# Performance work log

Measured on AMD Instinct MI355X. Metric: run time of the kernel, lower is better.

Reference implementation:

```python
import jax, jax.numpy as jnp
import numpy as np

NUM_EXPERTS = 8
HIDDEN = 1024
FFN = 2048
TOKENS = 2048


def setup_inputs() -> dict:
    key = jax.random.key(0)
    k_x, k_idx, k_w1, k_w2 = jax.random.split(key, 4)
    scale = 0.02
    x = jax.random.normal(k_x, (TOKENS, HIDDEN), dtype=jnp.float32)
    expert_indices = jax.random.randint(k_idx, (TOKENS,), 0, NUM_EXPERTS, dtype=jnp.int64)
    W1 = jax.random.normal(k_w1, (NUM_EXPERTS, HIDDEN, FFN), dtype=jnp.float32) * scale
    b1 = jnp.zeros((NUM_EXPERTS, FFN), dtype=jnp.float32)
    W2 = jax.random.normal(k_w2, (NUM_EXPERTS, FFN, HIDDEN), dtype=jnp.float32) * scale
    b2 = jnp.zeros((NUM_EXPERTS, HIDDEN), dtype=jnp.float32)
    return {"x": x, "expert_indices": expert_indices, "W1": W1, "b1": b1, "W2": W2, "b2": b2}


def reference(x, expert_indices, W1, b1, W2, b2):
    # Each token routed to one expert's MLP: Linear -> GELU(exact) -> Linear.
    # Dropout is identity in eval mode. Loop is over the small fixed expert set.
    out = jnp.zeros_like(x)
    for e in range(NUM_EXPERTS):
        h = jax.nn.gelu(x @ W1[e] + b1[e], approximate=False)  # [T, FFN]
        y = h @ W2[e] + b2[e]                                   # [T, H]
        mask = (expert_indices == e)[:, None]
        out = out + jnp.where(mask, y, 0.0)
    return out
```

## Files before the change

kernel.cpp:

```cpp
#include <hip/hip_runtime.h>

#define T_TOK 2048
#define HID   1024
#define FFN   2048
#define NEXP  8
#define MAX_SLOTS 40

typedef __attribute__((ext_vector_type(8))) short bf16x8;
typedef __attribute__((ext_vector_type(4))) float f32x4;

__device__ __forceinline__ short f2bf(float f) {
    unsigned u = __builtin_bit_cast(unsigned, f);
    u = (u + 0x7fffu + ((u >> 16) & 1u)) >> 16;
    return (short)u;
}

__device__ __forceinline__ float gelu_exact(float x) {
    return 0.5f * x * (1.0f + erff(x * 0.70710678118654752f));
}

__device__ __forceinline__ void async_cp16(const short* g, short* l) {
    __builtin_amdgcn_global_load_lds(
        (const __attribute__((address_space(1))) unsigned int*)g,
        (__attribute__((address_space(3))) unsigned int*)l, 16, 0, 0);
}

__device__ __forceinline__ void wtrans_body(
        const float* __restrict__ W, short* __restrict__ WT,
        int K, int N, int e, int kblk, int nblk) {
    int tid = threadIdx.x;
    int w = tid >> 6, l = tid & 63;
    int kb = kblk * 32 + w * 8;
    int n4 = nblk * 256 + l * 4;
    const float* src = W + (size_t)e * K * N + (size_t)kb * N + n4;
    float4 v[8];
#pragma unroll
    for (int r = 0; r < 8; r++)
        v[r] = *(const float4*)(src + (size_t)r * N);
    int kpanel = kb >> 6;
    int kc = (kb >> 3) & 7;
    int npanel = n4 >> 7;
    int n_in = n4 & 127;
    int kpanels = K >> 6;
    short* dst = WT + (size_t)e * K * N
               + ((size_t)npanel * kpanels + kpanel) * 8192
               + kc * 1024 + n_in * 8;
#pragma unroll
    for (int j = 0; j < 4; j++) {
        bf16x8 o = {f2bf(((const float*)&v[0])[j]), f2bf(((const float*)&v[1])[j]),
                    f2bf(((const float*)&v[2])[j]), f2bf(((const float*)&v[3])[j]),
                    f2bf(((const float*)&v[4])[j]), f2bf(((const float*)&v[5])[j]),
                    f2bf(((const float*)&v[6])[j]), f2bf(((const float*)&v[7])[j])};
        *(bf16x8*)(dst + j * 8) = o;
    }
}

__global__ __launch_bounds__(256) void prep_kernel(
        const float* __restrict__ x, const int* __restrict__ idx,
        const float* __restrict__ b2,
        const float* __restrict__ W1, const float* __restrict__ W2,
        short* __restrict__ xb, float* __restrict__ out,
        short* __restrict__ W1T, short* __restrict__ W2T,
        int* __restrict__ offs, int* __restrict__ cnts,
        int* __restrict__ tokl,
        int* __restrict__ slot_e, int* __restrict__ slot_t0) {
    int bx = blockIdx.x;
    int tid = threadIdx.x;
    if (bx < 2048) {
        int e = bx >> 8, rem = bx & 255;
        wtrans_body(W1, W1T, HID, FFN, e, rem & 31, rem >> 5);
    } else if (bx < 4096) {
        int b = bx - 2048;
        int e = b >> 8, rem = b & 255;
        wtrans_body(W2, W2T, FFN, HID, e, rem & 63, rem >> 6);
    } else if (bx < 5120) {
        int i = ((bx - 4096) * 256 + tid) * 8;
        float4 v0 = *(const float4*)(x + i);
        float4 v1 = *(const float4*)(x + i + 4);
        bf16x8 r = {f2bf(v0.x), f2bf(v0.y), f2bf(v0.z), f2bf(v0.w),
                    f2bf(v1.x), f2bf(v1.y), f2bf(v1.z), f2bf(v1.w)};
        *(bf16x8*)(xb + i) = r;
    } else if (bx < 7168) {
        int t = bx - 5120;
        int e = idx[t];
        ((float4*)(out + (size_t)t * HID))[tid] =
            ((const float4*)(b2 + (size_t)e * HID))[tid];
    } else {
        __shared__ int c[NEXP], cur[NEXP], o[NEXP];
        if (tid < NEXP) { c[tid] = 0; cur[tid] = 0; }
        __syncthreads();
        for (int t = tid; t < T_TOK; t += 256) atomicAdd(&c[idx[t]], 1);
        __syncthreads();
        if (tid == 0) {
            int s = 0;
            for (int e = 0; e < NEXP; e++) { o[e] = s; s += c[e]; }
            int ns = 0;
            for (int e = 0; e < NEXP; e++)
                for (int t0 = 0; t0 < c[e]; t0 += 64) {
                    slot_e[ns] = e; slot_t0[ns] = t0; ns++;
                }
            for (; ns < MAX_SLOTS; ns++) slot_e[ns] = -1;
        }
        __syncthreads();
        if (tid < NEXP) { offs[tid] = o[tid]; cnts[tid] = c[tid]; }
        for (int t = tid; t < T_TOK; t += 256) {
            int e = idx[t];
            int p = o[e] + atomicAdd(&cur[e], 1);
            tokl[p] = t;
        }
    }
}

__global__ __launch_bounds__(256) void gemm1_kernel(
        const short* __restrict__ xb, const short* __restrict__ W1T,
        const float* __restrict__ b1,
        const int* __restrict__ offs, const int* __restrict__ cnts,
        const int* __restrict__ tokl,
        const int* __restrict__ slot_e, const int* __restrict__ slot_t0,
        short* __restrict__ hg) {
    int s = blockIdx.y;
    int e = slot_e[s];
    if (e < 0) return;
    int t0 = slot_t0[s], count = cnts[e], off = offs[e];
    int n0 = blockIdx.x * 128;

    __shared__ short As[2 * 64 * 64];
    __shared__ short Bs[2 * 8 * 128 * 8];
    __shared__ int stok[64];

    int tid = threadIdx.x;
    if (tid < 64) {
        int p = t0 + tid;
        stok[tid] = tokl[off + (p < count ? p : count - 1)];
    }
    __syncthreads();

    int w = tid >> 6, l = tid & 63, l15 = l & 15, quad = l >> 4;
    int wm = (w >> 1) * 32, wn = (w & 1) * 64;

    int m0 = w * 16 + (l >> 3), m1 = m0 + 8;
    int cs = l & 7;
    int c0 = (cs - m0) & 7, c1 = (cs - m1) & 7;
    const short* gA0 = xb + (size_t)stok[m0] * HID + c0 * 8;
    const short* gA1 = xb + (size_t)stok[m1] * HID + c1 * 8;
    int aoff = w * 1024 + l * 8;

    const short* Bpan = W1T + (size_t)e * (HID * FFN)
                      + (size_t)(n0 >> 7) * ((HID >> 6) * 8192);
    int bo0 = (2 * w) * 1024 + l * 8;
    int bo1 = bo0 + 1024;
    int bo2 = bo0 + 512;
    int bo3 = bo1 + 512;

    auto stage = [&](int buf, int kt) {
        const short* bp = Bpan + (size_t)kt * 8192;
        short* As_b = As + buf * 4096;
        short* Bs_b = Bs + buf * 8192;
        async_cp16(gA0, As_b + aoff);
        async_cp16(gA1, As_b + aoff + 512);
        async_cp16(bp + bo0, Bs_b + bo0);
        async_cp16(bp + bo1, Bs_b + bo1);
        async_cp16(bp + bo2, Bs_b + bo2);
        async_cp16(bp + bo3, Bs_b + bo3);
        gA0 += 64; gA1 += 64;
    };

    f32x4 acc[2][4];
#pragma unroll
    for (int i = 0; i < 2; i++)
#pragma unroll
        for (int j = 0; j < 4; j++) acc[i][j] = (f32x4){0.f, 0.f, 0.f, 0.f};

    stage(0, 0);
    __syncthreads();

    const int KT = HID / 64;
    for (int kt = 0; kt < KT; kt++) {
        if (kt + 1 < KT) stage((kt + 1) & 1, kt + 1);
        const short* As_b = As + (kt & 1) * 4096;
        const short* Bs_b = Bs + (kt & 1) * 8192;
        bf16x8 a[2][2], b[2][4];
#pragma unroll
        for (int kk = 0; kk < 2; kk++) {
#pragma unroll
            for (int mt = 0; mt < 2; mt++) {
                int m = wm + mt * 16 + l15;
                a[kk][mt] = *(const bf16x8*)&As_b[m * 64 + (((kk * 4 + quad) + m) & 7) * 8];
            }
#pragma unroll
            for (int nt = 0; nt < 4; nt++) {
                int n = wn + nt * 16 + l15;
                b[kk][nt] = *(const bf16x8*)&Bs_b[(kk * 4 + quad) * 1024 + n * 8];
            }
        }
#pragma unroll
        for (int kk = 0; kk < 2; kk++)
#pragma unroll
            for (int mt = 0; mt < 2; mt++)
#pragma unroll
                for (int nt = 0; nt < 4; nt++)
                    acc[mt][nt] = __builtin_amdgcn_mfma_f32_16x16x32_bf16(
                        a[kk][mt], b[kk][nt], acc[mt][nt], 0, 0, 0);
        __syncthreads();
    }

    const float* b1e = b1 + e * FFN + n0;
#pragma unroll
    for (int mt = 0; mt < 2; mt++) {
        int rbase = wm + mt * 16 + quad * 4;
#pragma unroll
        for (int nt = 0; nt < 4; nt++) {
            int coln = wn + nt * 16 + l15;
            float bb = b1e[coln];
#pragma unroll
            for (int r = 0; r < 4; r++) {
                int p = t0 + rbase + r;
                if (p < count)
                    hg[(size_t)(off + p) * FFN + n0 + coln] =
                        f2bf(gelu_exact(acc[mt][nt][r] + bb));
            }
        }
    }
}

__global__ __launch_bounds__(256) void gemm2_kernel(
        const short* __restrict__ hg, const short* __restrict__ W2T,
        const int* __restrict__ offs, const int* __restrict__ cnts,
        const int* __restrict__ tokl,
        const int* __restrict__ slot_e, const int* __restrict__ slot_t0,
        float* __restrict__ out) {
    int s = blockIdx.y;
    int e = slot_e[s];
    if (e < 0) return;
    int t0 = slot_t0[s], count = cnts[e], off = offs[e];
    int ks = blockIdx.z;
    int n0 = blockIdx.x * 128;

    __shared__ short As[2 * 64 * 64];
    __shared__ short Bs[2 * 8 * 128 * 8];
    __shared__ int stok[64];

    int tid = threadIdx.x;
    if (tid < 64) {
        int p = t0 + tid;
        stok[tid] = tokl[off + (p < count ? p : count - 1)];
    }
    __syncthreads();

    int w = tid >> 6, l = tid & 63, l15 = l & 15, quad = l >> 4;
    int wm = (w >> 1) * 32, wn = (w & 1) * 64;

    int m0 = w * 16 + (l >> 3), m1 = m0 + 8;
    int cs = l & 7;
    int c0 = (cs - m0) & 7, c1 = (cs - m1) & 7;
    int g0 = off + (t0 + m0 < count ? t0 + m0 : count - 1);
    int g1 = off + (t0 + m1 < count ? t0 + m1 : count - 1);
    const short* gA0 = hg + (size_t)g0 * FFN + ks * 1024 + c0 * 8;
    const short* gA1 = hg + (size_t)g1 * FFN + ks * 1024 + c1 * 8;
    int aoff = w * 1024 + l * 8;

    const short* Bpan = W2T + (size_t)e * (FFN * HID)
                      + (size_t)(n0 >> 7) * ((FFN >> 6) * 8192)
                      + (size_t)ks * 16 * 8192;
    int bo0 = (2 * w) * 1024 + l * 8;
    int bo1 = bo0 + 1024;
    int bo2 = bo0 + 512;
    int bo3 = bo1 + 512;

    auto stage = [&](int buf, int kt) {
        const short* bp = Bpan + (size_t)kt * 8192;
        short* As_b = As + buf * 4096;
        short* Bs_b = Bs + buf * 8192;
        async_cp16(gA0, As_b + aoff);
        async_cp16(gA1, As_b + aoff + 512);
        async_cp16(bp + bo0, Bs_b + bo0);
        async_cp16(bp + bo1, Bs_b + bo1);
        async_cp16(bp + bo2, Bs_b + bo2);
        async_cp16(bp + bo3, Bs_b + bo3);
        gA0 += 64; gA1 += 64;
    };

    f32x4 acc[2][4];
#pragma unroll
    for (int i = 0; i < 2; i++)
#pragma unroll
        for (int j = 0; j < 4; j++) acc[i][j] = (f32x4){0.f, 0.f, 0.f, 0.f};

    stage(0, 0);
    __syncthreads();

    const int KT = 16;
    for (int kt = 0; kt < KT; kt++) {
        if (kt + 1 < KT) stage((kt + 1) & 1, kt + 1);
        const short* As_b = As + (kt & 1) * 4096;
        const short* Bs_b = Bs + (kt & 1) * 8192;
        bf16x8 a[2][2], b[2][4];
#pragma unroll
        for (int kk = 0; kk < 2; kk++) {
#pragma unroll
            for (int mt = 0; mt < 2; mt++) {
                int m = wm + mt * 16 + l15;
                a[kk][mt] = *(const bf16x8*)&As_b[m * 64 + (((kk * 4 + quad) + m) & 7) * 8];
            }
#pragma unroll
            for (int nt = 0; nt < 4; nt++) {
                int n = wn + nt * 16 + l15;
                b[kk][nt] = *(const bf16x8*)&Bs_b[(kk * 4 + quad) * 1024 + n * 8];
            }
        }
#pragma unroll
        for (int kk = 0; kk < 2; kk++)
#pragma unroll
            for (int mt = 0; mt < 2; mt++)
#pragma unroll
                for (int nt = 0; nt < 4; nt++)
                    acc[mt][nt] = __builtin_amdgcn_mfma_f32_16x16x32_bf16(
                        a[kk][mt], b[kk][nt], acc[mt][nt], 0, 0, 0);
        __syncthreads();
    }

#pragma unroll
    for (int mt = 0; mt < 2; mt++) {
        int rbase = wm + mt * 16 + quad * 4;
#pragma unroll
        for (int nt = 0; nt < 4; nt++) {
            int coln = n0 + wn + nt * 16 + l15;
#pragma unroll
            for (int r = 0; r < 4; r++) {
                int p = t0 + rbase + r;
                if (p < count) {
                    int tok = stok[rbase + r];
                    atomicAdd(out + (size_t)tok * HID + coln, acc[mt][nt][r]);
                }
            }
        }
    }
}

extern "C" void kernel_launch(void* const* d_in, const int* in_sizes, int n_in,
                              void* d_out, int out_size, void* d_ws, size_t ws_size,
                              hipStream_t stream) {
    const float* x   = (const float*)d_in[0];
    const int*   idx = (const int*)d_in[1];
    const float* W1  = (const float*)d_in[2];
    const float* b1  = (const float*)d_in[3];
    const float* W2  = (const float*)d_in[4];
    const float* b2  = (const float*)d_in[5];
    float* out = (float*)d_out;

    const size_t META = 32768;
    int*   offs    = (int*)d_ws;
    int*   cnts    = offs + 8;
    int*   tokl    = offs + 16;
    int*   slot_e  = offs + 16 + T_TOK;
    int*   slot_t0 = slot_e + MAX_SLOTS;
    char*  base    = (char*)d_ws + META;
    short* xb  = (short*)base;
    short* hg  = (short*)(base + (size_t)T_TOK * HID * 2);
    short* W1T = (short*)(base + (size_t)T_TOK * HID * 2 + (size_t)T_TOK * FFN * 2);
    short* W2T = W1T + (size_t)NEXP * FFN * HID;

    prep_kernel<<<7169, 256, 0, stream>>>(
        x, idx, b2, W1, W2, xb, out, W1T, W2T,
        offs, cnts, tokl, slot_e, slot_t0);

    gemm1_kernel<<<dim3(FFN / 128, MAX_SLOTS), 256, 0, stream>>>(
        xb, W1T, b1, offs, cnts, tokl, slot_e, slot_t0, hg);
    gemm2_kernel<<<dim3(HID / 128, MAX_SLOTS, 2), 256, 0, stream>>>(
        hg, W2T, offs, cnts, tokl, slot_e, slot_t0, out);
}
```

Baseline: 230.1 us.

## Pre-gather sorted tokens, overlap W2 conversion with GEMM1, relax pipeline waits

```diff
diff --git a/kernel.cpp b/kernel.cpp
--- a/kernel.cpp
+++ b/kernel.cpp
@@ -55,97 +55,103 @@
     }
 }
 
-__global__ __launch_bounds__(256) void prep_kernel(
-        const float* __restrict__ x, const int* __restrict__ idx,
-        const float* __restrict__ b2,
-        const float* __restrict__ W1, const float* __restrict__ W2,
-        short* __restrict__ xb, float* __restrict__ out,
-        short* __restrict__ W1T, short* __restrict__ W2T,
+__global__ __launch_bounds__(256) void bucket_kernel(
+        const int* __restrict__ idx,
         int* __restrict__ offs, int* __restrict__ cnts,
         int* __restrict__ tokl,
         int* __restrict__ slot_e, int* __restrict__ slot_t0) {
+    int tid = threadIdx.x;
+    __shared__ int c[NEXP], cur[NEXP], o[NEXP];
+    if (tid < NEXP) { c[tid] = 0; cur[tid] = 0; }
+    __syncthreads();
+    for (int t = tid; t < T_TOK; t += 256) atomicAdd(&c[idx[t]], 1);
+    __syncthreads();
+    if (tid == 0) {
+        int s = 0;
+        for (int e = 0; e < NEXP; e++) { o[e] = s; s += c[e]; }
+        int ns = 0;
+        for (int e = 0; e < NEXP; e++)
+            for (int t0 = 0; t0 < c[e]; t0 += 64) {
+                slot_e[ns] = e; slot_t0[ns] = t0; ns++;
+            }
+        for (; ns < MAX_SLOTS; ns++) slot_e[ns] = -1;
+    }
+    __syncthreads();
+    if (tid < NEXP) { offs[tid] = o[tid]; cnts[tid] = c[tid]; }
+    for (int t = tid; t < T_TOK; t += 256) {
+        int e = idx[t];
+        int p = o[e] + atomicAdd(&cur[e], 1);
+        tokl[p] = t;
+    }
+}
+
+__global__ __launch_bounds__(256) void prep_kernel(
+        const float* __restrict__ x, const int* __restrict__ idx,
+        const float* __restrict__ b2, const float* __restrict__ W1,
+        const int* __restrict__ tokl,
+        short* __restrict__ xb, float* __restrict__ out,
+        short* __restrict__ W1T) {
     int bx = blockIdx.x;
     int tid = threadIdx.x;
     if (bx < 2048) {
         int e = bx >> 8, rem = bx & 255;
         wtrans_body(W1, W1T, HID, FFN, e, rem & 31, rem >> 5);
-    } else if (bx < 4096) {
-        int b = bx - 2048;
-        int e = b >> 8, rem = b & 255;
-        wtrans_body(W2, W2T, FFN, HID, e, rem & 63, rem >> 6);
-    } else if (bx < 5120) {
-        int i = ((bx - 4096) * 256 + tid) * 8;
-        float4 v0 = *(const float4*)(x + i);
-        float4 v1 = *(const float4*)(x + i + 4);
+    } else if (bx < 3072) {
+        int p = (bx - 2048) * 2 + (tid >> 7);
+        int lane = tid & 127;
+        int tok = tokl[p];
+        const float* src = x + (size_t)tok * HID + lane * 8;
+        float4 v0 = *(const float4*)(src);
+        float4 v1 = *(const float4*)(src + 4);
         bf16x8 r = {f2bf(v0.x), f2bf(v0.y), f2bf(v0.z), f2bf(v0.w),
                     f2bf(v1.x), f2bf(v1.y), f2bf(v1.z), f2bf(v1.w)};
-        *(bf16x8*)(xb + i) = r;
-    } else if (bx < 7168) {
-        int t = bx - 5120;
+        *(bf16x8*)(xb + (size_t)p * HID + lane * 8) = r;
+    } else {
+        int t = bx - 3072;
         int e = idx[t];
         ((float4*)(out + (size_t)t * HID))[tid] =
             ((const float4*)(b2 + (size_t)e * HID))[tid];
-    } else {
-        __shared__ int c[NEXP], cur[NEXP], o[NEXP];
-        if (tid < NEXP) { c[tid] = 0; cur[tid] = 0; }
-        __syncthreads();
-        for (int t = tid; t < T_TOK; t += 256) atomicAdd(&c[idx[t]], 1);
-        __syncthreads();
-        if (tid == 0) {
-            int s = 0;
-            for (int e = 0; e < NEXP; e++) { o[e] = s; s += c[e]; }
-            int ns = 0;
-            for (int e = 0; e < NEXP; e++)
-                for (int t0 = 0; t0 < c[e]; t0 += 64) {
-                    slot_e[ns] = e; slot_t0[ns] = t0; ns++;
-                }
-            for (; ns < MAX_SLOTS; ns++) slot_e[ns] = -1;
-        }
-        __syncthreads();
-        if (tid < NEXP) { offs[tid] = o[tid]; cnts[tid] = c[tid]; }
-        for (int t = tid; t < T_TOK; t += 256) {
-            int e = idx[t];
-            int p = o[e] + atomicAdd(&cur[e], 1);
-            tokl[p] = t;
-        }
-    }
-}
-
-__global__ __launch_bounds__(256) void gemm1_kernel(
+    }
+}
+
+__global__ __launch_bounds__(256) void gemm1_w2_kernel(
         const short* __restrict__ xb, const short* __restrict__ W1T,
         const float* __restrict__ b1,
         const int* __restrict__ offs, const int* __restrict__ cnts,
-        const int* __restrict__ tokl,
         const int* __restrict__ slot_e, const int* __restrict__ slot_t0,
-        short* __restrict__ hg) {
-    int s = blockIdx.y;
+        short* __restrict__ hg,
+        const float* __restrict__ W2, short* __restrict__ W2T) {
+    __shared__ short As[2 * 64 * 64];
+    __shared__ short Bs[2 * 8 * 128 * 8];
+
+    int bx = blockIdx.x;
+    if (bx >= 640) {
+        int b = bx - 640;
+        int e = b >> 8, rem = b & 255;
+        wtrans_body(W2, W2T, FFN, HID, e, rem & 63, rem >> 6);
+        return;
+    }
+
+    int s = bx >> 4;
     int e = slot_e[s];
     if (e < 0) return;
     int t0 = slot_t0[s], count = cnts[e], off = offs[e];
-    int n0 = blockIdx.x * 128;
-
-    __shared__ short As[2 * 64 * 64];
-    __shared__ short Bs[2 * 8 * 128 * 8];
-    __shared__ int stok[64];
-
-    int tid = threadIdx.x;
-    if (tid < 64) {
-        int p = t0 + tid;
-        stok[tid] = tokl[off + (p < count ? p : count - 1)];
-    }
-    __syncthreads();
-
+    int n0 = (bx & 15) * 128;
+
+    int tid = threadIdx.x;
     int w = tid >> 6, l = tid & 63, l15 = l & 15, quad = l >> 4;
     int wm = (w >> 1) * 32, wn = (w & 1) * 64;
 
     int m0 = w * 16 + (l >> 3), m1 = m0 + 8;
     int cs = l & 7;
     int c0 = (cs - m0) & 7, c1 = (cs - m1) & 7;
-    const short* gA0 = xb + (size_t)stok[m0] * HID + c0 * 8;
-    const short* gA1 = xb + (size_t)stok[m1] * HID + c1 * 8;
+    int p0 = off + (t0 + m0 < count ? t0 + m0 : count - 1);
+    int p1 = off + (t0 + m1 < count ? t0 + m1 : count - 1);
+    const short* gA0 = xb + (size_t)p0 * HID + c0 * 8;
+    const short* gA1 = xb + (size_t)p1 * HID + c1 * 8;
     int aoff = w * 1024 + l * 8;
 
-    const short* Bpan = W1T + (size_t)e * (HID * FFN)
+    const short* Bpan = W1T + (size_t)e * (FFN * HID)
                       + (size_t)(n0 >> 7) * ((HID >> 6) * 8192);
     int bo0 = (2 * w) * 1024 + l * 8;
     int bo1 = bo0 + 1024;
@@ -156,13 +162,12 @@
         const short* bp = Bpan + (size_t)kt * 8192;
         short* As_b = As + buf * 4096;
         short* Bs_b = Bs + buf * 8192;
-        async_cp16(gA0, As_b + aoff);
-        async_cp16(gA1, As_b + aoff + 512);
+        async_cp16(gA0 + kt * 64, As_b + aoff);
+        async_cp16(gA1 + kt * 64, As_b + aoff + 512);
         async_cp16(bp + bo0, Bs_b + bo0);
         async_cp16(bp + bo1, Bs_b + bo1);
         async_cp16(bp + bo2, Bs_b + bo2);
         async_cp16(bp + bo3, Bs_b + bo3);
-        gA0 += 64; gA1 += 64;
     };
 
     f32x4 acc[2][4];
@@ -171,12 +176,18 @@
 #pragma unroll
         for (int j = 0; j < 4; j++) acc[i][j] = (f32x4){0.f, 0.f, 0.f, 0.f};
 
+    const int KT = HID / 64;
     stage(0, 0);
-    __syncthreads();
-
-    const int KT = HID / 64;
     for (int kt = 0; kt < KT; kt++) {
-        if (kt + 1 < KT) stage((kt + 1) & 1, kt + 1);
+        if (kt + 1 < KT) {
+            stage((kt + 1) & 1, kt + 1);
+            asm volatile("s_waitcnt vmcnt(6)" ::: "memory");
+        } else {
+            asm volatile("s_waitcnt vmcnt(0)" ::: "memory");
+        }
+        __builtin_amdgcn_sched_barrier(0);
+        __builtin_amdgcn_s_barrier();
+
         const short* As_b = As + (kt & 1) * 4096;
         const short* Bs_b = Bs + (kt & 1) * 8192;
         bf16x8 a[2][2], b[2][4];
@@ -201,7 +212,9 @@
                 for (int nt = 0; nt < 4; nt++)
                     acc[mt][nt] = __builtin_amdgcn_mfma_f32_16x16x32_bf16(
                         a[kk][mt], b[kk][nt], acc[mt][nt], 0, 0, 0);
-        __syncthreads();
+
+        __builtin_amdgcn_sched_barrier(0);
+        __builtin_amdgcn_s_barrier();
     }
 
     const float* b1e = b1 + e * FFN + n0;
@@ -238,15 +251,8 @@
 
     __shared__ short As[2 * 64 * 64];
     __shared__ short Bs[2 * 8 * 128 * 8];
-    __shared__ int stok[64];
-
-    int tid = threadIdx.x;
-    if (tid < 64) {
-        int p = t0 + tid;
-        stok[tid] = tokl[off + (p < count ? p : count - 1)];
-    }
-    __syncthreads();
-
+
+    int tid = threadIdx.x;
     int w = tid >> 6, l = tid & 63, l15 = l & 15, quad = l >> 4;
     int wm = (w >> 1) * 32, wn = (w & 1) * 64;
 
@@ -271,13 +277,12 @@
         const short* bp = Bpan + (size_t)kt * 8192;
         short* As_b = As + buf * 4096;
         short* Bs_b = Bs + buf * 8192;
-        async_cp16(gA0, As_b + aoff);
-        async_cp16(gA1, As_b + aoff + 512);
+        async_cp16(gA0 + kt * 64, As_b + aoff);
+        async_cp16(gA1 + kt * 64, As_b + aoff + 512);
         async_cp16(bp + bo0, Bs_b + bo0);
         async_cp16(bp + bo1, Bs_b + bo1);
         async_cp16(bp + bo2, Bs_b + bo2);
         async_cp16(bp + bo3, Bs_b + bo3);
-        gA0 += 64; gA1 += 64;
     };
 
     f32x4 acc[2][4];
@@ -286,12 +291,18 @@
 #pragma unroll
         for (int j = 0; j < 4; j++) acc[i][j] = (f32x4){0.f, 0.f, 0.f, 0.f};
 
+    const int KT = 16;
     stage(0, 0);
-    __syncthreads();
-
-    const int KT = 16;
     for (int kt = 0; kt < KT; kt++) {
-        if (kt + 1 < KT) stage((kt + 1) & 1, kt + 1);
+        if (kt + 1 < KT) {
+            stage((kt + 1) & 1, kt + 1);
+            asm volatile("s_waitcnt vmcnt(6)" ::: "memory");
+        } else {
+            asm volatile("s_waitcnt vmcnt(0)" ::: "memory");
+        }
+        __builtin_amdgcn_sched_barrier(0);
+        __builtin_amdgcn_s_barrier();
+
         const short* As_b = As + (kt & 1) * 4096;
         const short* Bs_b = Bs + (kt & 1) * 8192;
         bf16x8 a[2][2], b[2][4];
@@ -316,7 +327,9 @@
                 for (int nt = 0; nt < 4; nt++)
                     acc[mt][nt] = __builtin_amdgcn_mfma_f32_16x16x32_bf16(
                         a[kk][mt], b[kk][nt], acc[mt][nt], 0, 0, 0);
-        __syncthreads();
+
+        __builtin_amdgcn_sched_barrier(0);
+        __builtin_amdgcn_s_barrier();
     }
 
 #pragma unroll
@@ -329,7 +342,7 @@
             for (int r = 0; r < 4; r++) {
                 int p = t0 + rbase + r;
                 if (p < count) {
-                    int tok = stok[rbase + r];
+                    int tok = tokl[off + p];
                     atomicAdd(out + (size_t)tok * HID + coln, acc[mt][nt][r]);
                 }
             }
@@ -360,12 +373,14 @@
     short* W1T = (short*)(base + (size_t)T_TOK * HID * 2 + (size_t)T_TOK * FFN * 2);
     short* W2T = W1T + (size_t)NEXP * FFN * HID;
 
-    prep_kernel<<<7169, 256, 0, stream>>>(
-        x, idx, b2, W1, W2, xb, out, W1T, W2T,
-        offs, cnts, tokl, slot_e, slot_t0);
-
-    gemm1_kernel<<<dim3(FFN / 128, MAX_SLOTS), 256, 0, stream>>>(
-        xb, W1T, b1, offs, cnts, tokl, slot_e, slot_t0, hg);
+    bucket_kernel<<<1, 256, 0, stream>>>(idx, offs, cnts, tokl, slot_e, slot_t0);
+
+    prep_kernel<<<5120, 256, 0, stream>>>(
+        x, idx, b2, W1, tokl, xb, out, W1T);
+
+    gemm1_w2_kernel<<<2688, 256, 0, stream>>>(
+        xb, W1T, b1, offs, cnts, slot_e, slot_t0, hg, W2, W2T);
+
     gemm2_kernel<<<dim3(HID / 128, MAX_SLOTS, 2), 256, 0, stream>>>(
         hg, W2T, offs, cnts, tokl, slot_e, slot_t0, out);
 }
```

Measured after the change: 230.9 us. Within noise of the previous version (+0.4%).
